# Kernel tuning notes

Measured on AMD Instinct MI355X. Metric: run time of the kernel, lower is better.

Reference implementation:

```python
import jax, jax.numpy as jnp
import numpy as np


def _phi(x):
    # ELU(x) + 1 feature map (positive kernel feature map)
    return jax.nn.elu(x) + 1.0


def setup_inputs() -> dict:
    key = jax.random.key(0)
    k1, k2, k3 = jax.random.split(key, 3)
    B, S, E = 4, 4096, 1024
    inputs = jax.random.normal(k1, (B, S, E), dtype=jnp.float32)
    mask = jnp.ones((B, S), dtype=jnp.float32)
    w_qkv = jax.random.normal(k2, (3 * E, E), dtype=jnp.float32) * (E ** -0.5)
    b_qkv = jax.random.normal(k3, (3 * E,), dtype=jnp.float32) * 0.02
    return {"inputs": inputs, "mask": mask, "w_qkv": w_qkv, "b_qkv": b_qkv, "num_heads": 16}


def reference(inputs, mask, w_qkv, b_qkv, num_heads):
    B, S, E = inputs.shape
    H = num_heads
    D = E // H
    # qkv projection: torch Linear is x @ W.T + b
    qkv = inputs @ w_qkv.T + b_qkv                     # (B, S, 3E)
    qkv = qkv.reshape(B, S, 3, H, D)
    q = qkv[:, :, 0]                                   # (B, S, H, D)
    k = qkv[:, :, 1]
    v = qkv[:, :, 2]
    # key masking (float multiply, as in einsum 'bshd,bs->bshd')
    k = k * mask[:, :, None, None]
    kq = _phi(q)                                       # (B, S, H, D)
    kk = _phi(k)                                       # (B, S, H, D)
    # kv outer-product accumulation over sequence: (B, H, M, D)
    kv = jnp.einsum('bshd,bshm->bhmd', kk, v)
    # normalizer
    z = 1.0 / (jnp.einsum('bshd,bhd->bsh', kq, kk.sum(axis=1)) + 1e-6)
    # final contraction
    attn = jnp.einsum('bshd,bhmd,bsh->bshm', kq, kv, z)  # (B, S, H, D)
    attn = attn.reshape(B, S, E)
    # NOTE: original forward computes a projection but returns `attn` (dropout is
    # identity at inference), so projection is dead code and omitted here.
    return attn
```

## Files before the change

### kernel.cpp

```cpp
#include <hip/hip_runtime.h>

typedef unsigned short u16;
typedef short bf16x8 __attribute__((ext_vector_type(8)));
typedef float f32x4 __attribute__((ext_vector_type(4)));
typedef u16 u16x8 __attribute__((ext_vector_type(8)));
typedef u16 u16x4 __attribute__((ext_vector_type(4)));

#define B_ 4
#define S_ 4096
#define E_ 1024
#define H_ 16
#define D_ 64
#define M_ 16384
#define N_ 3072
#define K_ 1024

__device__ __forceinline__ u16 f2b(float f) {
    unsigned x = __builtin_bit_cast(unsigned, f);
    return (u16)((x + 0x7fffu + ((x >> 16) & 1u)) >> 16);
}
__device__ __forceinline__ float b2f(u16 u) {
    unsigned x = ((unsigned)u) << 16;
    return __builtin_bit_cast(float, x);
}
__device__ __forceinline__ float phi_f(float x) { return x > 0.f ? x + 1.f : __expf(x); }

__device__ __forceinline__ void gload16(const void* g, void* l) {
    __builtin_amdgcn_global_load_lds((const __attribute__((address_space(1))) void*)g,
                                     (__attribute__((address_space(3))) void*)l, 16, 0, 0);
}

#define MEMFENCE asm volatile("" ::: "memory")

__global__ void cvt_bf16(const float* __restrict__ in, u16* __restrict__ out, int n8) {
    int stride = gridDim.x * blockDim.x;
    for (int i = blockIdx.x * blockDim.x + threadIdx.x; i < n8; i += stride) {
        const float4* p = (const float4*)(in + (size_t)i * 8);
        float4 a = p[0], b = p[1];
        u16x8 o;
        o[0] = f2b(a.x); o[1] = f2b(a.y); o[2] = f2b(a.z); o[3] = f2b(a.w);
        o[4] = f2b(b.x); o[5] = f2b(b.y); o[6] = f2b(b.z); o[7] = f2b(b.w);
        *(u16x8*)(out + (size_t)i * 8) = o;
    }
}


__global__ __launch_bounds__(512, 2) void gemm_qkv(
    const u16* __restrict__ Abf, const u16* __restrict__ Wbf,
    const float* __restrict__ bias, const float* __restrict__ mask,
    u16* __restrict__ KQ, u16* __restrict__ KKT, u16* __restrict__ VT)
{
    __shared__ __align__(16) char lds[131072];

    int wg  = blockIdx.x;
    int xcd = wg & 7, ii = wg >> 3;
    int tm  = xcd * 8 + ii / 12;
    int tn  = ii % 12;
    int m0 = tm << 8, n0 = tn << 8;

    int t = threadIdx.x;
    int l = t & 63, wid = t >> 6;
    int wr = wid >> 2, wc = wid & 3;
    int lg = l >> 4, lr = l & 15;

    int srow  = t >> 3;
    int scolE = ((t & 7) ^ (srow & 7)) << 3;
    int t16   = t * 16;

    const u16* gA = Abf + (size_t)(m0 + srow) * K_ + scolE;
    const u16* gB = Wbf + (size_t)(n0 + srow) * K_ + scolE;

    const char* aB = lds + (wr * 128 + lr) * 128;
    const char* bB = lds + 32768 + (wc * 64 + lr) * 128;
    int pc0 = (lg * 16) ^ ((lr & 7) << 4);
    int pc1 = pc0 ^ 64;

    f32x4 acc[8][4] = {};
    bf16x8 av[4][2], bv2[2][2];

#define RD_A(BO, MI0) { _Pragma("unroll") for (int m_ = 0; m_ < 4; ++m_) { \
    av[m_][0] = *(const bf16x8*)(aB + (BO) + (MI0 + m_) * 2048 + pc0); \
    av[m_][1] = *(const bf16x8*)(aB + (BO) + (MI0 + m_) * 2048 + pc1); } }

#define RD_B(BO, NI0) { _Pragma("unroll") for (int n_ = 0; n_ < 2; ++n_) { \
    bv2[n_][0] = *(const bf16x8*)(bB + (BO) + (NI0 + n_) * 2048 + pc0); \
    bv2[n_][1] = *(const bf16x8*)(bB + (BO) + (NI0 + n_) * 2048 + pc1); } }

#define ST_A(TT, HI, BO) { \
    gload16(gA + (size_t)((HI) * 64) * K_ + (TT) * 64, lds + (BO) + (HI) * 8192 + t16); \
    gload16(gA + (size_t)((HI) * 64 + 128) * K_ + (TT) * 64, lds + (BO) + 16384 + (HI) * 8192 + t16); }

#define ST_B(TT, PR, BO) { \
    gload16(gB + (size_t)((PR) * 128) * K_ + (TT) * 64, lds + (BO) + 32768 + (PR) * 16384 + t16); \
    gload16(gB + (size_t)((PR) * 128 + 64) * K_ + (TT) * 64, lds + (BO) + 32768 + (PR) * 16384 + 8192 + t16); }

#define BAR { MEMFENCE; __builtin_amdgcn_s_barrier(); MEMFENCE; }

#define MM(MI0, NI0) { __builtin_amdgcn_s_setprio(1); \
    _Pragma("unroll") for (int m_ = 0; m_ < 4; ++m_) \
    _Pragma("unroll") for (int n_ = 0; n_ < 2; ++n_) \
    _Pragma("unroll") for (int h_ = 0; h_ < 2; ++h_) \
        acc[(MI0) + m_][(NI0) + n_] = __builtin_amdgcn_mfma_f32_16x16x32_bf16( \
            av[m_][h_], bv2[n_][h_], acc[(MI0) + m_][(NI0) + n_], 0, 0, 0); \
    __builtin_amdgcn_s_setprio(0); }

    ST_A(0, 0, 0); ST_A(0, 1, 0); ST_B(0, 0, 0); ST_B(0, 1, 0);
    ST_A(1, 0, 65536); ST_A(1, 1, 65536);
    asm volatile("s_waitcnt vmcnt(4)" ::: "memory");
    __builtin_amdgcn_s_barrier();
    MEMFENCE;

#pragma unroll 1
    for (int kt = 0; kt < 16; kt += 2) {
        int tp2 = kt + 2 < 16 ? kt + 2 : 15;
        int tp3 = kt + 3 < 16 ? kt + 3 : 15;
        RD_A(0, 0); RD_B(0, 0); ST_B(kt + 1, 0, 65536); BAR; MM(0, 0); BAR;
        RD_B(0, 2); ST_B(kt + 1, 1, 65536); BAR; MM(0, 2); BAR;
        RD_A(0, 4); ST_A(tp2, 0, 0); BAR; MM(4, 2); BAR;
        RD_B(0, 0); ST_A(tp2, 1, 0);
        asm volatile("s_waitcnt vmcnt(4)" ::: "memory");
        BAR; MM(4, 0); BAR;
        RD_A(65536, 0); RD_B(65536, 0); ST_B(tp2, 0, 0); BAR; MM(0, 0); BAR;
        RD_B(65536, 2); ST_B(tp2, 1, 0); BAR; MM(0, 2); BAR;
        RD_A(65536, 4); ST_A(tp3, 0, 65536); BAR; MM(4, 2); BAR;
        RD_B(65536, 0); ST_A(tp3, 1, 65536);
        asm volatile("s_waitcnt vmcnt(4)" ::: "memory");
        BAR; MM(4, 0); BAR;
    }

    int part = n0 >> 10;

    float bv[4];
#pragma unroll
    for (int ni = 0; ni < 4; ++ni) bv[ni] = bias[n0 + wc * 64 + ni * 16 + lr];

    if (part == 0) {
#pragma unroll
        for (int mi = 0; mi < 8; ++mi)
#pragma unroll
            for (int j = 0; j < 4; ++j) {
                int row = m0 + wr * 128 + mi * 16 + lg * 4 + j;
#pragma unroll
                for (int ni = 0; ni < 4; ++ni) {
                    int col = n0 + wc * 64 + ni * 16 + lr;
                    KQ[(size_t)row * E_ + col] = f2b(phi_f(acc[mi][ni][j] + bv[ni]));
                }
            }
    } else {
        u16* dst0 = (part == 1) ? KKT : VT;
        int b  = m0 >> 12;
        int sl = m0 & (S_ - 1);
        int h  = ((tn & 3) << 2) | wc;
#pragma unroll
        for (int mi = 0; mi < 8; ++mi) {
            int sbase = sl + wr * 128 + mi * 16 + lg * 4;
            float mk[4];
#pragma unroll
            for (int j = 0; j < 4; ++j)
                mk[j] = (part == 1) ? mask[m0 + wr * 128 + mi * 16 + lg * 4 + j] : 1.f;
#pragma unroll
            for (int ni = 0; ni < 4; ++ni) {
                u16x4 o;
#pragma unroll
                for (int j = 0; j < 4; ++j) {
                    float v = acc[mi][ni][j] + bv[ni];
                    if (part == 1) v = phi_f(v * mk[j]);
                    o[j] = f2b(v);
                }
                int d = ni * 16 + lr;
                *(u16x4*)(dst0 + ((size_t)((b * H_ + h) * D_ + d)) * S_ + sbase) = o;
            }
        }
    }
}

__global__ __launch_bounds__(256) void kv_ksum_partial(
    const u16* __restrict__ VT, const u16* __restrict__ KKT,
    float* __restrict__ KVP, float* __restrict__ KSP)
{
    __shared__ __align__(16) u16 smem[8192];
    u16* As = smem;
    u16* Bs = smem + 4096;
    int bh = blockIdx.x;
    int ch = blockIdx.y;
    int s0 = ch << 8;
    int t = threadIdx.x;
    int l = t & 63, w = t >> 6;
    int lg = l >> 4, lr = l & 15;
    const u16* Ag = VT + (size_t)bh * (D_ * S_);
    const u16* Bg = KKT + (size_t)bh * (D_ * S_);
    int srow = t >> 3, scol = (t & 7) << 3;

    f32x4 acc[4] = {};
    float ks = 0.f;
    int kd = t >> 2;
    int kq4 = (t & 3) << 4;

    for (int kt = 0; kt < 4; ++kt) {
        __syncthreads();
        int sb = s0 + kt * 64;
#pragma unroll
        for (int i = 0; i < 2; ++i) {
            gload16(Ag + (size_t)(srow + i * 32) * S_ + sb + scol, As + i * 2048 + t * 8);
            gload16(Bg + (size_t)(srow + i * 32) * S_ + sb + scol, Bs + i * 2048 + t * 8);
        }
        __syncthreads();
#pragma unroll
        for (int i = 0; i < 16; ++i) ks += b2f(Bs[kd * 64 + kq4 + i]);
#pragma unroll
        for (int kh = 0; kh < 2; ++kh) {
            int ko = kh * 32 + lg * 8;
            bf16x8 a = *(const bf16x8*)&As[(w * 16 + lr) * 64 + ko];
#pragma unroll
            for (int ni = 0; ni < 4; ++ni) {
                bf16x8 bb = *(const bf16x8*)&Bs[(ni * 16 + lr) * 64 + ko];
                acc[ni] = __builtin_amdgcn_mfma_f32_16x16x32_bf16(a, bb, acc[ni], 0, 0, 0);
            }
        }
    }
    float* kvp = KVP + (size_t)ch * (64 * 4096) + bh * 4096;
#pragma unroll
    for (int ni = 0; ni < 4; ++ni)
#pragma unroll
        for (int j = 0; j < 4; ++j)
            kvp[(w * 16 + lg * 4 + j) * 64 + ni * 16 + lr] = acc[ni][j];
    ks += __shfl_xor(ks, 1);
    ks += __shfl_xor(ks, 2);
    if ((t & 3) == 0) KSP[ch * 4096 + bh * 64 + kd] = ks;
}

__global__ void reduce_kv(const float* __restrict__ KVP, const float* __restrict__ KSP,
                          float* __restrict__ KV, float* __restrict__ KSUM)
{
    int g = blockIdx.x * 256 + threadIdx.x;
#pragma unroll 1
    for (int i = g * 4; i < g * 4 + 4; ++i) {
        float s = 0.f;
#pragma unroll
        for (int c = 0; c < 16; ++c) s += KVP[(size_t)c * (64 * 4096) + i];
        KV[i] = s;
    }
    if (g < 4096) {
        float s = 0.f;
#pragma unroll
        for (int c = 0; c < 16; ++c) s += KSP[c * 4096 + g];
        KSUM[g] = s;
    }
}

__global__ __launch_bounds__(256) void attn_out(
    const u16* __restrict__ KQ, const float* __restrict__ KV,
    const float* __restrict__ KSUM, float* __restrict__ Out)
{
    __shared__ __align__(16) u16 kqs[16384];
    __shared__ __align__(16) u16 bsm[5120];
    __shared__ float den[256];
    int bh = blockIdx.x, ch = blockIdx.y;
    int b = bh >> 4, h = bh & 15;
    int t = threadIdx.x;
    int l = t & 63, w = t >> 6;
    int lg = l >> 4, lr = l & 15;
    size_t row0 = (size_t)b * S_ + ch * 256;
    int srow = t >> 3, scol = (t & 7) << 3;
#pragma unroll
    for (int i = 0; i < 8; ++i)
        gload16(KQ + (row0 + srow + i * 32) * E_ + h * 64 + scol, kqs + i * 2048 + t * 8);

    const float* kvg = KV + bh * 4096;
#pragma unroll
    for (int ii = 0; ii < 16; ii += 4) {
        float4 v = *(const float4*)(kvg + t * 16 + ii);
        u16x4 o; o[0] = f2b(v.x); o[1] = f2b(v.y); o[2] = f2b(v.z); o[3] = f2b(v.w);
        *(u16x4*)&bsm[t * 16 + ii] = o;
    }
    if (t < 64) bsm[4096 + t] = f2b(KSUM[bh * 64 + t]);
    for (int i = t; i < 960; i += 256) bsm[4160 + i] = 0;
    __syncthreads();

    f32x4 acc[4][5] = {};
#pragma unroll
    for (int kh = 0; kh < 2; ++kh) {
        int ko = kh * 32 + lg * 8;
        bf16x8 af[4];
#pragma unroll
        for (int mi = 0; mi < 4; ++mi)
            af[mi] = *(const bf16x8*)&kqs[(w * 64 + mi * 16 + lr) * 64 + ko];
#pragma unroll
        for (int ni = 0; ni < 5; ++ni) {
            bf16x8 bb = *(const bf16x8*)&bsm[(ni * 16 + lr) * 64 + ko];
#pragma unroll
            for (int mi = 0; mi < 4; ++mi)
                acc[mi][ni] = __builtin_amdgcn_mfma_f32_16x16x32_bf16(af[mi], bb, acc[mi][ni], 0, 0, 0);
        }
    }
    if (lr == 0) {
#pragma unroll
        for (int mi = 0; mi < 4; ++mi)
#pragma unroll
            for (int j = 0; j < 4; ++j)
                den[w * 64 + mi * 16 + lg * 4 + j] = acc[mi][4][j];
    }
    __syncthreads();
#pragma unroll
    for (int mi = 0; mi < 4; ++mi)
#pragma unroll
        for (int j = 0; j < 4; ++j) {
            int sl = w * 64 + mi * 16 + lg * 4 + j;
            float z = 1.f / (den[sl] + 1e-6f);
            float* op = Out + (row0 + sl) * E_ + h * 64;
#pragma unroll
            for (int ni = 0; ni < 4; ++ni)
                op[ni * 16 + lr] = acc[mi][ni][j] * z;
        }
}

extern "C" void kernel_launch(void* const* d_in, const int* in_sizes, int n_in,
                              void* d_out, int out_size, void* d_ws, size_t ws_size,
                              hipStream_t stream)
{
    const float* inputs = (const float*)d_in[0];
    const float* mask   = (const float*)d_in[1];
    const float* w_qkv  = (const float*)d_in[2];
    const float* b_qkv  = (const float*)d_in[3];

    u16* Abf = (u16*)d_ws;
    u16* Wbf = Abf + (size_t)M_ * K_;
    u16* KQ  = Wbf + (size_t)N_ * K_;
    float* KVP  = (float*)(KQ + (size_t)M_ * E_);
    float* KSP  = KVP + 16 * 64 * 4096;
    float* KV   = KSP + 16 * 4096;
    float* KSUM = KV + 64 * 4096;

    u16* KKT = (u16*)d_out;
    u16* VT  = KKT + (size_t)M_ * E_;

    cvt_bf16<<<2048, 256, 0, stream>>>(inputs, Abf, M_ * K_ / 8);
    cvt_bf16<<<768, 256, 0, stream>>>(w_qkv, Wbf, N_ * K_ / 8);
    gemm_qkv<<<768, 512, 0, stream>>>(Abf, Wbf, b_qkv, mask, KQ, KKT, VT);
    kv_ksum_partial<<<dim3(64, 16), 256, 0, stream>>>(VT, KKT, KVP, KSP);
    reduce_kv<<<256, 256, 0, stream>>>(KVP, KSP, KV, KSUM);
    attn_out<<<dim3(64, 16), 256, 0, stream>>>(KQ, KV, KSUM, (float*)d_out);
}
```

Measured before the change: 168.1 us.

## Keep both B fragment halves in registers and halve barriers in GEMM pipeline

Splits the B-fragment registers into two sets (columns 0-1 and 2-3) so the fourth MFMA phase reuses the already-loaded b01 instead of re-reading B from LDS. It also drops the second barrier in each phase, adding an explicit lgkmcnt(0) wait plus a sched_barrier, and reorders which A/B global-to-LDS prefetches are issued in each phase. The aim is fewer LDS reads and fewer workgroup barriers per K step. In exchange it uses more VGPRs and depends on the reordered prefetch schedule staying race-free with only one barrier per phase.

```diff
diff --git a/kernel.cpp b/kernel.cpp
--- a/kernel.cpp
+++ b/kernel.cpp
@@ -76,15 +76,19 @@
     int pc1 = pc0 ^ 64;
 
     f32x4 acc[8][4] = {};
-    bf16x8 av[4][2], bv2[2][2];
+    bf16x8 av[4][2], b01[2][2], b23[2][2];
 
 #define RD_A(BO, MI0) { _Pragma("unroll") for (int m_ = 0; m_ < 4; ++m_) { \
     av[m_][0] = *(const bf16x8*)(aB + (BO) + (MI0 + m_) * 2048 + pc0); \
     av[m_][1] = *(const bf16x8*)(aB + (BO) + (MI0 + m_) * 2048 + pc1); } }
 
-#define RD_B(BO, NI0) { _Pragma("unroll") for (int n_ = 0; n_ < 2; ++n_) { \
-    bv2[n_][0] = *(const bf16x8*)(bB + (BO) + (NI0 + n_) * 2048 + pc0); \
-    bv2[n_][1] = *(const bf16x8*)(bB + (BO) + (NI0 + n_) * 2048 + pc1); } }
+#define RD_B01(BO) { _Pragma("unroll") for (int n_ = 0; n_ < 2; ++n_) { \
+    b01[n_][0] = *(const bf16x8*)(bB + (BO) + n_ * 2048 + pc0); \
+    b01[n_][1] = *(const bf16x8*)(bB + (BO) + n_ * 2048 + pc1); } }
+
+#define RD_B23(BO) { _Pragma("unroll") for (int n_ = 0; n_ < 2; ++n_) { \
+    b23[n_][0] = *(const bf16x8*)(bB + (BO) + (2 + n_) * 2048 + pc0); \
+    b23[n_][1] = *(const bf16x8*)(bB + (BO) + (2 + n_) * 2048 + pc1); } }
 
 #define ST_A(TT, HI, BO) { \
     gload16(gA + (size_t)((HI) * 64) * K_ + (TT) * 64, lds + (BO) + (HI) * 8192 + t16); \
@@ -95,17 +99,19 @@
     gload16(gB + (size_t)((PR) * 128 + 64) * K_ + (TT) * 64, lds + (BO) + 32768 + (PR) * 16384 + 8192 + t16); }
 
 #define BAR { MEMFENCE; __builtin_amdgcn_s_barrier(); MEMFENCE; }
-
-#define MM(MI0, NI0) { __builtin_amdgcn_s_setprio(1); \
+#define LGKM0 { asm volatile("s_waitcnt lgkmcnt(0)" ::: "memory"); \
+                __builtin_amdgcn_sched_barrier(0); }
+
+#define MM16(MI0, NI0, BV) { __builtin_amdgcn_s_setprio(1); \
     _Pragma("unroll") for (int m_ = 0; m_ < 4; ++m_) \
     _Pragma("unroll") for (int n_ = 0; n_ < 2; ++n_) \
     _Pragma("unroll") for (int h_ = 0; h_ < 2; ++h_) \
         acc[(MI0) + m_][(NI0) + n_] = __builtin_amdgcn_mfma_f32_16x16x32_bf16( \
-            av[m_][h_], bv2[n_][h_], acc[(MI0) + m_][(NI0) + n_], 0, 0, 0); \
+            av[m_][h_], BV[n_][h_], acc[(MI0) + m_][(NI0) + n_], 0, 0, 0); \
     __builtin_amdgcn_s_setprio(0); }
 
-    ST_A(0, 0, 0); ST_A(0, 1, 0); ST_B(0, 0, 0); ST_B(0, 1, 0);
-    ST_A(1, 0, 65536); ST_A(1, 1, 65536);
+    ST_A(0, 0, 0); ST_B(0, 0, 0); ST_B(0, 1, 0); ST_A(0, 1, 0);
+    ST_A(1, 0, 65536); ST_B(1, 0, 65536);
     asm volatile("s_waitcnt vmcnt(4)" ::: "memory");
     __builtin_amdgcn_s_barrier();
     MEMFENCE;
@@ -114,18 +120,24 @@
     for (int kt = 0; kt < 16; kt += 2) {
         int tp2 = kt + 2 < 16 ? kt + 2 : 15;
         int tp3 = kt + 3 < 16 ? kt + 3 : 15;
-        RD_A(0, 0); RD_B(0, 0); ST_B(kt + 1, 0, 65536); BAR; MM(0, 0); BAR;
-        RD_B(0, 2); ST_B(kt + 1, 1, 65536); BAR; MM(0, 2); BAR;
-        RD_A(0, 4); ST_A(tp2, 0, 0); BAR; MM(4, 2); BAR;
-        RD_B(0, 0); ST_A(tp2, 1, 0);
+        RD_A(0, 0); RD_B01(0); ST_A(kt + 1, 1, 65536);
+        BAR; LGKM0; MM16(0, 0, b01);
+        RD_B23(0); ST_B(kt + 1, 1, 65536);
+        BAR; LGKM0; MM16(0, 2, b23);
+        RD_A(0, 4); ST_A(tp2, 0, 0);
+        BAR; LGKM0; MM16(4, 2, b23);
+        ST_B(tp2, 0, 0);
         asm volatile("s_waitcnt vmcnt(4)" ::: "memory");
-        BAR; MM(4, 0); BAR;
-        RD_A(65536, 0); RD_B(65536, 0); ST_B(tp2, 0, 0); BAR; MM(0, 0); BAR;
-        RD_B(65536, 2); ST_B(tp2, 1, 0); BAR; MM(0, 2); BAR;
-        RD_A(65536, 4); ST_A(tp3, 0, 65536); BAR; MM(4, 2); BAR;
-        RD_B(65536, 0); ST_A(tp3, 1, 65536);
+        BAR; LGKM0; MM16(4, 0, b01);
+        RD_A(65536, 0); RD_B01(65536); ST_A(tp2, 1, 0);
+        BAR; LGKM0; MM16(0, 0, b01);
+        RD_B23(65536); ST_B(tp2, 1, 0);
+        BAR; LGKM0; MM16(0, 2, b23);
+        RD_A(65536, 4); ST_A(tp3, 0, 65536);
+        BAR; LGKM0; MM16(4, 2, b23);
+        ST_B(tp3, 0, 65536);
         asm volatile("s_waitcnt vmcnt(4)" ::: "memory");
-        BAR; MM(4, 0); BAR;
+        BAR; LGKM0; MM16(4, 0, b01);
     }
 
     int part = n0 >> 10;
```

Result: slower. 171.9 us (+2.2%).
